# Kernel tuning notes

Hardware: AMD Instinct MI355X
Metric: run time of the kernel (lower is better)

Reference implementation:

```python
import jax, jax.numpy as jnp
import numpy as np

INPUT_SIZE = 512.0
NMS_THRESH = 0.3
SCORE_THRESH = 0.5
TOPC = 256        # candidates entering NMS (top-scoring above-threshold boxes)
MAX_DETS = 32     # py_cpu_nms(...)[:32]


def conv3x3(x, w):
    return jax.lax.conv_general_dilated(x, w, (1, 1), 'SAME',
                                        dimension_numbers=('NCHW', 'OIHW', 'NCHW'))


def bn_eval(x, g, b, m, v, eps=1e-5):
    inv = g * jax.lax.rsqrt(v + eps)
    return x * inv[None, :, None, None] + (b - m * inv)[None, :, None, None]


def lrelu(x):
    return jnp.where(x >= 0, x, 0.01 * x)


def upsample2x(x):  # F.interpolate(scale_factor=2), default nearest
    return jnp.repeat(jnp.repeat(x, 2, axis=2), 2, axis=3)


def fpn_head(x, hw1, hg1, hb1, hm1, hv1, hw2, hg2, hb2, hm2, hv2):
    x = lrelu(bn_eval(conv3x3(x, hw1), hg1, hb1, hm1, hv1))
    x = lrelu(bn_eval(conv3x3(x, hw2), hg2, hb2, hm2, hv2))
    return x


def decode_boxes(t, a):
    # inverse of coordinate_change: x1 = ax1 + tx*aw, w = aw*exp(tw)
    aw = a[:, 2] - a[:, 0]
    ah = a[:, 3] - a[:, 1]
    x1 = a[:, 0] + t[:, 0] * aw
    y1 = a[:, 1] + t[:, 1] * ah
    bw = aw * jnp.exp(t[:, 2])
    bh = ah * jnp.exp(t[:, 3])
    return jnp.stack([x1, y1, x1 + bw, y1 + bh], axis=1)


def pairwise_iou_p1(b):
    # py_cpu_nms convention: +1 in widths/areas
    x1, y1, x2, y2 = b[:, 0], b[:, 1], b[:, 2], b[:, 3]
    areas = (x2 - x1 + 1.0) * (y2 - y1 + 1.0)
    xx1 = jnp.maximum(x1[:, None], x1[None, :])
    yy1 = jnp.maximum(y1[:, None], y1[None, :])
    xx2 = jnp.minimum(x2[:, None], x2[None, :])
    yy2 = jnp.minimum(y2[:, None], y2[None, :])
    inter = jnp.maximum(0.0, xx2 - xx1 + 1.0) * jnp.maximum(0.0, yy2 - yy1 + 1.0)
    return inter / (areas[:, None] + areas[None, :] - inter)


def nms_keep(boxes, valid):
    # boxes pre-sorted by descending score; greedy suppression
    ovr = pairwise_iou_p1(boxes)
    idxs = jnp.arange(boxes.shape[0])

    def body(i, keep):
        sup = (ovr[i] > NMS_THRESH) & (idxs > i) & keep[i]
        return keep & ~sup

    return jax.lax.fori_loop(0, boxes.shape[0], body, valid)


def roi_adaptive_maxpool(feat, c):
    # feat [C,h,w]; c = [x1,y1,x2,y2] int32 feature-map coords
    # faithful F.adaptive_max_pool2d(feat[:, y1:y2, x1:x2], (7,7))
    C, h, w = feat.shape
    neg = jnp.finfo(feat.dtype).min

    def bin_masks(lo, hi, n_axis):
        L = hi - lo
        i = jnp.arange(7)
        start = (i * L) // 7
        end = ((i + 1) * L + 6) // 7  # ceil
        rel = jnp.arange(n_axis) - lo
        return (rel[None, :] >= start[:, None]) & (rel[None, :] < end[:, None])

    my = bin_masks(c[1], c[3], h)  # [7,h]
    mx = bin_masks(c[0], c[2], w)  # [7,w]
    rows = jnp.stack([jnp.max(jnp.where(my[i][None, :, None], feat, neg), axis=1)
                      for i in range(7)])                    # [7y,C,w]
    cols = jnp.stack([jnp.max(jnp.where(mx[j][None, None, :], rows, neg), axis=2)
                      for j in range(7)])
    return cols.transpose(2, 1, 0)


def rpn_level(feat, anchors, stride, clsw, locw):
    B = feat.shape[0]
    score = jax.nn.sigmoid(conv3x3(feat, clsw)).transpose(0, 2, 3, 1).reshape(B, -1)
    loc = conv3x3(feat, locw).transpose(0, 2, 3, 1).reshape(B, -1, 4)

    def per_image(f, sc, t):
        boxes = jnp.clip(decode_boxes(t, anchors), 0.0, INPUT_SIZE)
        bw = boxes[:, 2] - boxes[:, 0]
        bh = boxes[:, 3] - boxes[:, 1]
        valid = (sc > SCORE_THRESH) & (bw >= 2.0 * stride) & (bh >= 2.0 * stride)
        vals, idx = jax.lax.top_k(jnp.where(valid, sc, -1.0), TOPC)
        cb = boxes[idx]
        # original NMS ran on detached numpy -> stop_gradient
        keep = nms_keep(jax.lax.stop_gradient(cb), vals > SCORE_THRESH)
        order = jnp.argsort(jnp.where(keep, 0, 1), stable=True)[:MAX_DETS]
        m = keep[order]
        b32 = cb[order]
        s32 = vals[order]
        coords = jnp.where(m[:, None], b32.astype(jnp.int32) // stride,
                           jnp.array([0, 0, 2, 2], jnp.int32))
        pooled = jax.vmap(lambda cc: roi_adaptive_maxpool(f, cc))(coords)
        pooled = jnp.where(m[:, None, None, None], pooled, 0.0)
        dets = jnp.where(m[:, None], jnp.concatenate([b32, s32[:, None]], axis=1), 0.0)
        return dets, m, pooled

    return jax.vmap(per_image)(feat, score, loc)


def net_forward(layer2, layer3, layer4, anchors2, anchors3, anchors4,
                hw1, hg1, hb1, hm1, hv1, hw2, hg2, hb2, hm2, hv2, clsw, locw):
    head = (hw1, hg1, hb1, hm1, hv1, hw2, hg2, hb2, hm2, hv2)
    l3 = layer3 + upsample2x(layer4)
    l2 = layer2 + upsample2x(l3)
    f2 = fpn_head(l2, *head)
    f3 = fpn_head(l3, *head)
    f4 = fpn_head(layer4, *head)
    outs = [rpn_level(f, a, s, clsw, locw)
            for f, a, s in ((f2, anchors2, 8), (f3, anchors3, 16), (f4, anchors4, 32))]
    dets = jnp.stack([o[0] for o in outs], axis=1)  # [B,3,32,5] padded eval_test
    mask = jnp.stack([o[1] for o in outs], axis=1)  # [B,3,32] validity of each det
    rois = jnp.stack([o[2] for o in outs], axis=1)  # [B,3,32,256,7,7]
    return dets, mask, rois


def setup_inputs() -> dict:
    key = jax.random.key(0)
    ks = jax.random.split(key, 16)
    f32 = jnp.float32

    def n(k, shape, s=1.0):
        return jax.random.normal(k, shape, f32) * s

    S = 512

    def anchors_for(st):
        h = S // st
        c = (jnp.arange(h, dtype=f32) + 0.5) * st
        sz = jnp.array([4.0, 6.0, 8.0], f32) * st
        cy = jnp.broadcast_to(c[:, None, None], (h, h, 3))
        cx = jnp.broadcast_to(c[None, :, None], (h, h, 3))
        ss = jnp.broadcast_to(sz[None, None, :], (h, h, 3))
        return jnp.stack([cx - ss / 2, cy - ss / 2, cx + ss / 2, cy + ss / 2], -1).reshape(-1, 4)

    return {
        'layer2': n(ks[0], (2, 256, 64, 64)),
        'layer3': n(ks[1], (2, 256, 32, 32)),
        'layer4': n(ks[2], (2, 256, 16, 16)),
        'anchors2': anchors_for(8),
        'anchors3': anchors_for(16),
        'anchors4': anchors_for(32),
        'hw1': n(ks[3], (256, 256, 3, 3), 0.03),
        'hg1': 1.0 + n(ks[4], (256,), 0.1),
        'hb1': n(ks[5], (256,), 0.1),
        'hm1': n(ks[6], (256,), 0.1),
        'hv1': jax.random.uniform(ks[7], (256,), f32, 0.5, 1.5),
        'hw2': n(ks[8], (256, 256, 3, 3), 0.03),
        'hg2': 1.0 + n(ks[9], (256,), 0.1),
        'hb2': n(ks[10], (256,), 0.1),
        'hm2': n(ks[11], (256,), 0.1),
        'hv2': jax.random.uniform(ks[12], (256,), f32, 0.5, 1.5),
        'clsw': n(ks[13], (3, 256, 3, 3), 0.03),
        'locw': n(ks[14], (12, 256, 3, 3), 0.01),
    }


def reference(layer2, layer3, layer4, anchors2, anchors3, anchors4,
              hw1, hg1, hb1, hm1, hv1, hw2, hg2, hb2, hm2, hv2, clsw, locw):
    return net_forward(layer2, layer3, layer4, anchors2, anchors3, anchors4,
                       hw1, hg1, hb1, hm1, hv1, hw2, hg2, hb2, hm2, hv2, clsw, locw)
```

## Files before the change

kernel.cpp:

```cpp
#include <hip/hip_runtime.h>
#include <math.h>

typedef __attribute__((ext_vector_type(8))) _Float16 f16x8;
typedef __attribute__((ext_vector_type(16))) float f32x16;
typedef unsigned long long ull;

__device__ __forceinline__ void split2(float v, _Float16& h, _Float16& l) {
  h = (_Float16)v;
  l = (_Float16)((v - (float)h) * 4096.0f);
}

#define OFF_W1H  0UL
#define OFF_W1L  1179648UL
#define OFF_W2H  2359296UL
#define OFF_W2L  3538944UL
#define OFF_WRH  4718592UL
#define OFF_WRL  4866048UL
#define OFF_I0H  5013504UL
#define OFF_I0L  9207808UL
#define OFF_I1H  13402112UL
#define OFF_I1L  14450688UL
#define OFF_I2H  15499264UL
#define OFF_I2L  15761408UL
#define OFF_L3F  16023552UL
#define OFF_H0H  18120704UL
#define OFF_H0L  22315008UL
#define OFF_H1H  26509312UL
#define OFF_H1L  27557888UL
#define OFF_H2H  28606464UL
#define OFF_H2L  28868608UL
#define OFF_LOGITS 29130752UL
#define OFF_TVALS  29259776UL
#define OFF_SKEY   29775872UL
#define OFF_COORDS 29904896UL
#define OFF_BN     29908992UL
#define OFF_HIST   29917184UL
#define OFF_P0     29966336UL
#define WS_NEED2   51986432UL


__global__ __launch_bounds__(256) void zero_hist_kernel(unsigned int* __restrict__ hist)
{
  hist[blockIdx.x * 256 + threadIdx.x] = 0u;
}

#define L1SZ 589824
#define RPNSZ 73728
__global__ __launch_bounds__(256) void prep_w_kernel(
    const float* __restrict__ hw1, const float* __restrict__ hw2,
    const float* __restrict__ clsw, const float* __restrict__ locw,
    const float* __restrict__ hg1, const float* __restrict__ hb1,
    const float* __restrict__ hm1, const float* __restrict__ hv1,
    const float* __restrict__ hg2, const float* __restrict__ hb2,
    const float* __restrict__ hm2, const float* __restrict__ hv2,
    char* __restrict__ ws)
{
  if (blockIdx.x == 0) {
    int t = threadIdx.x;
    float* inv1 = (float*)(ws + OFF_BN);
    float* beta1 = inv1 + 256;
    float* inv2 = inv1 + 512;
    float* beta2 = inv1 + 768;
    float i1 = (float)((double)hg1[t] / sqrt((double)hv1[t] + 1e-5));
    inv1[t] = i1;
    beta1[t] = hb1[t] - hm1[t] * i1;
    float i2 = (float)((double)hg2[t] / sqrt((double)hv2[t] + 1e-5));
    inv2[t] = i2;
    beta2[t] = hb2[t] - hm2[t] * i2;
  }
  _Float16* w1h = (_Float16*)(ws + OFF_W1H);
  _Float16* w1l = (_Float16*)(ws + OFF_W1L);
  _Float16* w2h = (_Float16*)(ws + OFF_W2H);
  _Float16* w2l = (_Float16*)(ws + OFF_W2L);
  _Float16* wrh = (_Float16*)(ws + OFF_WRH);
  _Float16* wrl = (_Float16*)(ws + OFF_WRL);
  const int TOT = 2 * L1SZ + RPNSZ;
  for (int e = blockIdx.x * 256 + threadIdx.x; e < TOT; e += gridDim.x * 256) {
    float val; _Float16 *dh, *dl; int di;
    if (e < L1SZ) {
      int dydx = e >> 16, oc = (e >> 8) & 255, ic = e & 255;
      val = hw1[(size_t)(oc * 256 + ic) * 9 + dydx];
      dh = w1h; dl = w1l; di = e;
    } else if (e < 2 * L1SZ) {
      int e2 = e - L1SZ;
      int dydx = e2 >> 16, oc = (e2 >> 8) & 255, ic = e2 & 255;
      val = hw2[(size_t)(oc * 256 + ic) * 9 + dydx];
      dh = w2h; dl = w2l; di = e2;
    } else {
      int e3 = e - 2 * L1SZ;
      int dydx = e3 >> 13, oc = (e3 >> 8) & 31, ic = e3 & 255;
      if (oc < 3) val = clsw[(size_t)(oc * 256 + ic) * 9 + dydx];
      else if (oc < 15) val = locw[(size_t)((oc - 3) * 256 + ic) * 9 + dydx];
      else val = 0.f;
      dh = wrh; dl = wrl; di = e3;
    }
    _Float16 h, l;
    split2(val, h, l);
    dh[di] = h; dl[di] = l;
  }
}

__global__ __launch_bounds__(256) void fuse_kernel(
    const float* __restrict__ a, const float* __restrict__ bUp,
    float* __restrict__ f32chw, _Float16* __restrict__ oH, _Float16* __restrict__ oL,
    int H, int logW)
{
  __shared__ float T[32][65];
  int HW = H * H;
  int img = blockIdx.y;
  const float* ap = a + (size_t)img * 256 * HW;
  const float* bp = bUp ? (bUp + (size_t)img * 256 * (HW >> 2)) : nullptr;
  float* fp = f32chw ? (f32chw + (size_t)img * 256 * HW) : nullptr;
  _Float16* oHp = oH + (size_t)img * HW * 256;
  _Float16* oLp = oL + (size_t)img * HW * 256;
  int p0 = blockIdx.x * 64;
  int tid = threadIdx.x;
  int px = tid & 63, cg = tid >> 6;
  int gp = p0 + px;
  int y = gp >> logW, x = gp & (H - 1);
  int px2 = tid >> 2, q = tid & 3;
  for (int c0 = 0; c0 < 256; c0 += 32) {
    #pragma unroll
    for (int cc = 0; cc < 8; ++cc) {
      int c = c0 + cg * 8 + cc;
      float v = ap[(size_t)c * HW + gp];
      if (bp) v += bp[(size_t)c * (HW >> 2) + (y >> 1) * (H >> 1) + (x >> 1)];
      if (fp) fp[(size_t)c * HW + gp] = v;
      T[cg * 8 + cc][px] = v;
    }
    __syncthreads();
    {
      size_t oa = (size_t)(p0 + px2) * 256 + c0 + q * 8;
      f16x8 hs, ls;
      #pragma unroll
      for (int j = 0; j < 8; ++j) {
        float v = T[q * 8 + j][px2];
        _Float16 h, l;
        split2(v, h, l);
        hs[j] = h; ls[j] = l;
      }
      *(f16x8*)&oHp[oa] = hs;
      *(f16x8*)&oLp[oa] = ls;
    }
    __syncthreads();
  }
}

struct CArgs {
  const _Float16* inH[3]; const _Float16* inL[3];
  const _Float16* wH; const _Float16* wL;
  _Float16* outH[3]; _Float16* outL[3];
  const float* inv; const float* beta;
  float* logits; float* tvals;
  float* pbase; size_t pstride;
  int mode; int parts;
};

#define PXS 42

template<int OCW, int WN, int NI>
__global__ __launch_bounds__(WN * 64, 2) void conv_mfma_kernel(CArgs a)
{
  constexpr int NT = WN * 64;
  constexpr int NOC = WN * NI * 32;
  constexpr int OCG = OCW / NOC;
  __shared__ _Float16 Ph[2][100 * PXS], Pl[2][100 * PXS];

  int bt = blockIdx.x;
  int lvl, tile;
  if (bt < 64) { lvl = 0; tile = bt; }
  else if (bt < 80) { lvl = 1; tile = bt - 64; }
  else { lvl = 2; tile = bt - 80; }
  int H = (lvl == 0) ? 64 : ((lvl == 1) ? 32 : 16);
  int HW = H * H;
  int tpr = H >> 3;
  int ty0 = (tile / tpr) * 8, tx0 = (tile % tpr) * 8;
  int img = blockIdx.z;

  int part = blockIdx.y / OCG;
  int ocb = (blockIdx.y % OCG) * NOC;
  int nicb = 8 / a.parts;
  int icb0 = part * nicb;
  float* pout = (a.parts > 1) ? (a.pbase + (size_t)part * a.pstride) : nullptr;

  const _Float16* inH = a.inH[lvl] + (size_t)img * HW * 256;
  const _Float16* inL = a.inL[lvl] + (size_t)img * HW * 256;

  int tid = threadIdx.x;
  int lane = tid & 63, wn = tid >> 6;
  int row = lane & 31, khalf = lane >> 5;
  int abase[2];
  #pragma unroll
  for (int mi = 0; mi < 2; ++mi) {
    int m = mi * 32 + row;
    abase[mi] = ((m >> 3) * 10 + (m & 7)) * PXS + khalf * 8;
  }

  const _Float16* wHb = a.wH + (size_t)(ocb + wn * NI * 32 + row) * 256 + khalf * 8 + icb0 * 32;
  const _Float16* wLb = a.wL + (size_t)(ocb + wn * NI * 32 + row) * 256 + khalf * 8 + icb0 * 32;

  f32x16 acc1[2][NI], acc2[2][NI];
  #pragma unroll
  for (int mi = 0; mi < 2; ++mi)
    #pragma unroll
    for (int ni = 0; ni < NI; ++ni)
      #pragma unroll
      for (int j = 0; j < 16; ++j) { acc1[mi][ni][j] = 0.f; acc2[mi][ni][j] = 0.f; }

  auto stage = [&](int icb, int buf) {
    for (int u = tid; u < 400; u += NT) {
      int pxl = u >> 2, icq = u & 3;
      int py = pxl / 10, pxx = pxl - py * 10;
      int gy = ty0 + py - 1, gx = tx0 + pxx - 1;
      int lo = pxl * PXS + icq * 8;
      if ((unsigned)gy < (unsigned)H && (unsigned)gx < (unsigned)H) {
        size_t ga = (size_t)(gy * H + gx) * 256 + icb * 32 + icq * 8;
        *(f16x8*)&Ph[buf][lo] = *(const f16x8*)&inH[ga];
        *(f16x8*)&Pl[buf][lo] = *(const f16x8*)&inL[ga];
      } else {
        f16x8 z;
        #pragma unroll
        for (int j = 0; j < 8; ++j) z[j] = (_Float16)0.f;
        *(f16x8*)&Ph[buf][lo] = z;
        *(f16x8*)&Pl[buf][lo] = z;
      }
    }
  };

  stage(icb0, 0);
  __syncthreads();

  for (int rel = 0; rel < nicb; ++rel) {
    int cur = rel & 1;
    if (rel < nicb - 1) stage(icb0 + rel + 1, cur ^ 1);
    #pragma unroll
    for (int dydx = 0; dydx < 9; ++dydx) {
      int sh = ((dydx / 3) * 10 + (dydx % 3)) * PXS;
      #pragma unroll
      for (int k2 = 0; k2 < 2; ++k2) {
        f16x8 bh[NI], bl[NI], ah[2], al[2];
        #pragma unroll
        for (int ni = 0; ni < NI; ++ni) {
          size_t ga = (size_t)dydx * OCW * 256 + (size_t)ni * 32 * 256 + rel * 32 + k2 * 16;
          bh[ni] = *(const f16x8*)&wHb[ga];
          bl[ni] = *(const f16x8*)&wLb[ga];
        }
        #pragma unroll
        for (int mi = 0; mi < 2; ++mi) {
          int off = abase[mi] + sh + k2 * 16;
          ah[mi] = *(const f16x8*)&Ph[cur][off];
          al[mi] = *(const f16x8*)&Pl[cur][off];
        }
        __builtin_amdgcn_s_setprio(1);
        #pragma unroll
        for (int mi = 0; mi < 2; ++mi)
          #pragma unroll
          for (int ni = 0; ni < NI; ++ni) {
            acc1[mi][ni] = __builtin_amdgcn_mfma_f32_32x32x16_f16(ah[mi], bh[ni], acc1[mi][ni], 0, 0, 0);
            acc2[mi][ni] = __builtin_amdgcn_mfma_f32_32x32x16_f16(ah[mi], bl[ni], acc2[mi][ni], 0, 0, 0);
            acc2[mi][ni] = __builtin_amdgcn_mfma_f32_32x32x16_f16(al[mi], bh[ni], acc2[mi][ni], 0, 0, 0);
          }
        __builtin_amdgcn_s_setprio(0);
      }
    }
    __syncthreads();
  }

  int poffv = (lvl == 0) ? 0 : ((lvl == 1) ? 4096 : 5120);
  #pragma unroll
  for (int mi = 0; mi < 2; ++mi)
    #pragma unroll
    for (int ni = 0; ni < NI; ++ni) {
      int oc = ocb + wn * NI * 32 + ni * 32 + row;
      float v[16];
      #pragma unroll
      for (int r = 0; r < 16; ++r) v[r] = acc1[mi][ni][r] + acc2[mi][ni][r] * (1.f / 4096.f);
      if (pout) {
        float* pp = pout + (size_t)(img * 5376 + poffv) * OCW;
        #pragma unroll
        for (int r = 0; r < 16; ++r) {
          int ml = (r & 3) + 8 * (r >> 2) + 4 * khalf;
          int m = mi * 32 + ml;
          int y = ty0 + (m >> 3), x = tx0 + (m & 7);
          pp[(size_t)(y * H + x) * OCW + oc] = v[r];
        }
      } else if (a.mode == 0) {
        _Float16* outH = a.outH[lvl] + (size_t)img * HW * 256;
        _Float16* outL = a.outL[lvl] + (size_t)img * HW * 256;
        float iv = a.inv[oc], bb = a.beta[oc];
        #pragma unroll
        for (int r = 0; r < 16; ++r) {
          int ml = (r & 3) + 8 * (r >> 2) + 4 * khalf;
          int m = mi * 32 + ml;
          int y = ty0 + (m >> 3), x = tx0 + (m & 7);
          float vv = v[r] * iv + bb;
          vv = (vv >= 0.f) ? vv : 0.01f * vv;
          _Float16 h, l;
          split2(vv, h, l);
          size_t oa = (size_t)(y * H + x) * 256 + oc;
          outH[oa] = h;
          outL[oa] = l;
        }
      } else {
        if (oc < 15) {
          int abse = (lvl == 0) ? 0 : ((lvl == 1) ? 12288 : 15360);
          #pragma unroll
          for (int r = 0; r < 16; ++r) {
            int ml = (r & 3) + 8 * (r >> 2) + 4 * khalf;
            int m = mi * 32 + ml;
            int y = ty0 + (m >> 3), x = tx0 + (m & 7);
            int gi = img * 16128 + abse + (y * H + x) * 3;
            if (oc < 3) a.logits[gi + oc] = v[r];
            else { int r2 = oc - 3; a.tvals[(size_t)(gi + (r2 >> 2)) * 4 + (r2 & 3)] = v[r]; }
          }
        }
      }
    }
}

__global__ __launch_bounds__(256) void combine_head_kernel(
    const float* __restrict__ pb, int nparts,
    const float* __restrict__ inv, const float* __restrict__ beta,
    _Float16* __restrict__ oH0, _Float16* __restrict__ oL0,
    _Float16* __restrict__ oH1, _Float16* __restrict__ oL1,
    _Float16* __restrict__ oH2, _Float16* __restrict__ oL2)
{
  const size_t PS = 10752UL * 256UL;
  int g = blockIdx.x * 256 + threadIdx.x;
  int pixel = g >> 5, q = g & 31;
  size_t base = (size_t)pixel * 256 + q * 8;
  int img = pixel / 5376, rem = pixel - img * 5376;
  int lvl = (rem < 4096) ? 0 : ((rem < 5120) ? 1 : 2);
  int poffv = (lvl == 0) ? 0 : ((lvl == 1) ? 4096 : 5120);
  int HW = (lvl == 0) ? 4096 : ((lvl == 1) ? 1024 : 256);
  int lpx = rem - poffv;
  size_t oa = ((size_t)img * HW + lpx) * 256 + q * 8;
  _Float16* oH = ((lvl == 0) ? oH0 : ((lvl == 1) ? oH1 : oH2)) + oa;
  _Float16* oL = ((lvl == 0) ? oL0 : ((lvl == 1) ? oL1 : oL2)) + oa;
  f16x8 hs, ls;
  #pragma unroll
  for (int j = 0; j < 8; ++j) {
    int oc = q * 8 + j;
    float s = 0.f;
    for (int k = 0; k < nparts; ++k) s += pb[(size_t)k * PS + base + j];
    float vv = s * inv[oc] + beta[oc];
    vv = (vv >= 0.f) ? vv : 0.01f * vv;
    _Float16 h, l;
    split2(vv, h, l);
    hs[j] = h; ls[j] = l;
  }
  *(f16x8*)oH = hs;
  *(f16x8*)oL = ls;
}

__global__ __launch_bounds__(256) void combine_rpn_kernel(
    const float* __restrict__ praw, int nparts,
    float* __restrict__ logits, float* __restrict__ tvals)
{
  int g = blockIdx.x * 256 + threadIdx.x;
  int px = g >> 4, oc = g & 15;
  if (oc == 15) return;
  float s = 0.f;
  for (int p = 0; p < nparts; ++p) s += praw[((size_t)p * 10752 + px) * 32 + oc];
  int img = px / 5376, rem = px - img * 5376;
  int lvl = (rem < 4096) ? 0 : ((rem < 5120) ? 1 : 2);
  int poffv = (lvl == 0) ? 0 : ((lvl == 1) ? 4096 : 5120);
  int abase = (lvl == 0) ? 0 : ((lvl == 1) ? 12288 : 15360);
  int gi = img * 16128 + abase + (rem - poffv) * 3;
  if (oc < 3) logits[gi + oc] = s;
  else { int r2 = oc - 3; tvals[(size_t)(gi + (r2 >> 2)) * 4 + (r2 & 3)] = s; }
}

__device__ __forceinline__ void decode_one(const float* __restrict__ anch,
                                           const float* __restrict__ tv, int i,
                                           float& x1, float& y1, float& x2, float& y2)
{
  float t0 = tv[i * 4 + 0], t1 = tv[i * 4 + 1], t2 = tv[i * 4 + 2], t3 = tv[i * 4 + 3];
  float a0 = anch[i * 4 + 0], a1 = anch[i * 4 + 1], a2 = anch[i * 4 + 2], a3 = anch[i * 4 + 3];
  float aw = a2 - a0, ah = a3 - a1;
  float xx = a0 + t0 * aw;
  float yy = a1 + t1 * ah;
  float bw = aw * expf(t2);
  float bh = ah * expf(t3);
  x1 = fminf(fmaxf(xx, 0.f), 512.f);
  y1 = fminf(fmaxf(yy, 0.f), 512.f);
  x2 = fminf(fmaxf(xx + bw, 0.f), 512.f);
  y2 = fminf(fmaxf(yy + bh, 0.f), 512.f);
}

__global__ __launch_bounds__(256) void score_kernel(
    const float* __restrict__ logits, const float* __restrict__ tvals,
    const float* __restrict__ anch0, const float* __restrict__ anch1, const float* __restrict__ anch2,
    unsigned int* __restrict__ skey, unsigned int* __restrict__ hist)
{
  int g = blockIdx.x * 256 + threadIdx.x;
  if (g >= 2 * 16128) return;
  int img = g / 16128, r = g - img * 16128;
  int lvl = (r < 12288) ? 0 : ((r < 15360) ? 1 : 2);
  int abase = (lvl == 0) ? 0 : ((lvl == 1) ? 12288 : 15360);
  int stride = (lvl == 0) ? 8 : ((lvl == 1) ? 16 : 32);
  const float* anch = (lvl == 0) ? anch0 : ((lvl == 1) ? anch1 : anch2);
  int i = r - abase;
  float lv = logits[g];
  float sc = 1.f / (1.f + expf(-lv));
  float x1, y1, x2, y2;
  decode_one(anch, tvals + (size_t)(img * 16128 + abase) * 4, i, x1, y1, x2, y2);
  float minsz = 2.0f * (float)stride;
  bool valid = (sc > 0.5f) && ((x2 - x1) >= minsz) && ((y2 - y1) >= minsz);
  unsigned int key = valid ? __float_as_uint(sc) : 0u;
  skey[g] = key;
  if (valid)
    atomicAdd(&hist[(img * 3 + lvl) * 2048 + ((key & 0xFFFFFFu) >> 13)], 1u);
}

__global__ __launch_bounds__(256) void postproc_kernel(
    const float* __restrict__ tvals,
    const float* __restrict__ anch0, const float* __restrict__ anch1, const float* __restrict__ anch2,
    const unsigned int* __restrict__ skey, const unsigned int* __restrict__ hist,
    float* __restrict__ dout, int* __restrict__ coords)
{
  int lvl = blockIdx.x, img = blockIdx.y;
  int N = (lvl == 0) ? 12288 : ((lvl == 1) ? 3072 : 768);
  int stride = (lvl == 0) ? 8 : ((lvl == 1) ? 16 : 32);
  int abase = (lvl == 0) ? 0 : ((lvl == 1) ? 12288 : 15360);
  const float* anch = (lvl == 0) ? anch0 : ((lvl == 1) ? anch1 : anch2);
  const float* tv = tvals + (size_t)(img * 16128 + abase) * 4;
  const unsigned int* sk = skey + img * 16128 + abase;
  int tx = threadIdx.x;

  __shared__ int tot[256];
  __shared__ int sh_bin, sh_V;
  __shared__ ull slist[1024];
  __shared__ int scnt;
  __shared__ ull skey64[256];
  __shared__ float bx0[256], bx1[256], bx2[256], bx3[256], bar[256], bsc[256];
  __shared__ ull colT[256][4];
  __shared__ ull kinit[4], kfin[4];
  __shared__ unsigned char bkeepArr[256];
  __shared__ int sel[32];

  const unsigned int* hp = hist + (img * 3 + lvl) * 2048;
  unsigned int hloc[8];
  #pragma unroll
  for (int j = 0; j < 8; ++j) hloc[j] = hp[tx * 8 + j];
  int sl[9]; sl[8] = 0;
  #pragma unroll
  for (int j = 7; j >= 0; --j) sl[j] = sl[j + 1] + (int)hloc[j];
  tot[tx] = sl[0];
  if (tx == 0) { sh_bin = 2048; scnt = 0; }
  __syncthreads();
  int T = 0;
  for (int b = 0; b < 256; ++b) T += (b > tx) ? tot[b] : 0;
  if (tx == 0) sh_V = T + sl[0];
  __syncthreads();
  int V = sh_V;
  int needed = (V < 256) ? V : 256;
  if (needed > 0) {
    #pragma unroll
    for (int j = 0; j < 8; ++j) {
      int suf = T + sl[j];
      int sufn = (j < 7) ? (T + sl[j + 1]) : T;
      if (suf >= needed && sufn < needed) sh_bin = tx * 8 + j;
    }
  }
  #pragma unroll
  for (int q = 0; q < 4; ++q) slist[tx + q * 256] = 0ull;
  __syncthreads();
  int Bstar = sh_bin;

  if (needed > 0) {
    const uint4* sk4 = (const uint4*)sk;
    for (int i4 = tx; i4 < (N >> 2); i4 += 256) {
      uint4 v4 = sk4[i4];
      unsigned int vv[4] = {v4.x, v4.y, v4.z, v4.w};
      #pragma unroll
      for (int q = 0; q < 4; ++q) {
        unsigned int v = vv[q];
        if (v != 0u && (int)((v & 0xFFFFFFu) >> 13) >= Bstar) {
          int p = atomicAdd(&scnt, 1);
          if (p < 1024)
            slist[p] = ((ull)v << 32) | (ull)(0xFFFFFFFFu - (unsigned)(i4 * 4 + q));
        }
      }
    }
  }
  __syncthreads();
  int M = scnt < 1024 ? scnt : 1024;

  skey64[tx] = 0ull;
  __syncthreads();
  for (int it = tx; it < M; it += 256) {
    ull K = slist[it];
    int rank = 0;
    for (int j = 0; j < M; ++j) rank += (slist[j] > K) ? 1 : 0;
    if (rank < 256) skey64[rank] = K;
  }
  __syncthreads();

  {
    ull key = skey64[tx];
    float x1 = 0.f, y1 = 0.f, x2 = 0.f, y2 = 0.f, sc = 0.f;
    if (key != 0ull) {
      sc = __uint_as_float((unsigned int)(key >> 32));
      int idx = (int)(0xFFFFFFFFu - (unsigned int)(key & 0xFFFFFFFFull));
      decode_one(anch, tv, idx, x1, y1, x2, y2);
    }
    bx0[tx] = x1; bx1[tx] = y1; bx2[tx] = x2; bx3[tx] = y2;
    bsc[tx] = sc;
    bar[tx] = (x2 - x1 + 1.f) * (y2 - y1 + 1.f);
    ull b = __ballot(sc > 0.5f);
    if ((tx & 63) == 0) kinit[tx >> 6] = b;
  }
  __syncthreads();

  {
    float xj1 = bx0[tx], yj1 = bx1[tx], xj2 = bx2[tx], yj2 = bx3[tx], aj = bar[tx];
    #pragma unroll
    for (int w = 0; w < 4; ++w) {
      ull rr = 0ull;
      int j0 = w * 64;
      int ie = (tx < j0 + 64) ? tx : (j0 + 64);
      for (int i = j0; i < ie; ++i) {
        float xx1 = fmaxf(xj1, bx0[i]);
        float yy1 = fmaxf(yj1, bx1[i]);
        float xx2 = fminf(xj2, bx2[i]);
        float yy2 = fminf(yj2, bx3[i]);
        float ww = fmaxf(0.f, xx2 - xx1 + 1.f);
        float hh = fmaxf(0.f, yy2 - yy1 + 1.f);
        float inter = ww * hh;
        float ovr = inter / (aj + bar[i] - inter);
        rr |= (ovr > 0.3f) ? (1ull << (i & 63)) : 0ull;
      }
      colT[tx][w] = rr;
    }
  }
  __syncthreads();

  if (tx < 64) {
    int l = tx;
    ull cm[4][4];
    #pragma unroll
    for (int c = 0; c < 4; ++c)
      #pragma unroll
      for (int w = 0; w < 4; ++w) cm[c][w] = colT[l + 64 * c][w];
    int av[4];
    #pragma unroll
    for (int c = 0; c < 4; ++c) av[c] = (int)((kinit[c] >> l) & 1ull);
    for (int cw = 0; cw < 4; ++cw) {
      ull rem = __ballot(av[cw] != 0);
      while (rem) {
        int ib = __builtin_ctzll(rem);
        #pragma unroll
        for (int c = 0; c < 4; ++c) {
          int sup = (int)((cm[c][cw] >> ib) & 1ull);
          av[c] &= sup ^ 1;
        }
        ull ready = __ballot(av[cw] != 0);
        rem = (ib == 63) ? 0ull : (ready & (~0ull << (ib + 1)));
      }
    }
    #pragma unroll
    for (int c = 0; c < 4; ++c) {
      ull bw = __ballot(av[c] != 0);
      if (l == 0) kfin[c] = bw;
      bkeepArr[l + 64 * c] = (unsigned char)av[c];
    }
  }
  __syncthreads();

  {
    int r = tx;
    int m = bkeepArr[r];
    int K = 0, before = 0;
    #pragma unroll
    for (int c = 0; c < 4; ++c) {
      int pc = __popcll(kfin[c]);
      K += pc;
      if (r >= (c + 1) * 64) before += pc;
      else if (r > c * 64) before += __popcll(kfin[c] & ((1ull << (r - c * 64)) - 1ull));
    }
    int rank = m ? before : (K + r - before);
    if (rank < 32) sel[rank] = r;
  }
  __syncthreads();

  if (tx < 32) {
    int r = sel[tx];
    int m = bkeepArr[r];
    int ob = (img * 3 + lvl) * 32 + tx;
    float d0 = 0.f, d1 = 0.f, d2 = 0.f, d3 = 0.f, d4 = 0.f;
    int c0 = 0, c1 = 0, c2 = 2, c3 = 2;
    if (m) {
      d0 = bx0[r]; d1 = bx1[r]; d2 = bx2[r]; d3 = bx3[r]; d4 = bsc[r];
      c0 = ((int)d0) / stride; c1 = ((int)d1) / stride;
      c2 = ((int)d2) / stride; c3 = ((int)d3) / stride;
    }
    dout[ob * 5 + 0] = d0; dout[ob * 5 + 1] = d1; dout[ob * 5 + 2] = d2;
    dout[ob * 5 + 3] = d3; dout[ob * 5 + 4] = d4;
    dout[960 + ob] = m ? 1.f : 0.f;
    coords[ob * 5 + 0] = c0; coords[ob * 5 + 1] = c1;
    coords[ob * 5 + 2] = c2; coords[ob * 5 + 3] = c3;
    coords[ob * 5 + 4] = m;
  }
}

__global__ __launch_bounds__(256) void roipool_kernel(
    const _Float16* __restrict__ fh0, const _Float16* __restrict__ fl0,
    const _Float16* __restrict__ fh1, const _Float16* __restrict__ fl1,
    const _Float16* __restrict__ fh2, const _Float16* __restrict__ fl2,
    const int* __restrict__ coords, float* __restrict__ dout)
{
  int bx = blockIdx.x;
  int slot = bx / 49, bin = bx - slot * 49;
  int yi = bin / 7, xi = bin - yi * 7;
  int lvl = blockIdx.y, img = blockIdx.z;
  int ob = (img * 3 + lvl) * 32 + slot;
  int c = threadIdx.x;
  const int* cw = coords + ob * 5;
  float* outp = dout + 1152 + (size_t)ob * 256 * 49 + (size_t)c * 49 + yi * 7 + xi;
  int m = cw[4];
  if (!m) { *outp = 0.f; return; }
  int H = (lvl == 0) ? 64 : ((lvl == 1) ? 32 : 16);
  const _Float16* fh = ((lvl == 0) ? fh0 : ((lvl == 1) ? fh1 : fh2)) + (size_t)img * H * H * 256;
  const _Float16* fl = ((lvl == 0) ? fl0 : ((lvl == 1) ? fl1 : fl2)) + (size_t)img * H * H * 256;
  int lox = cw[0], loy = cw[1], hix = cw[2], hiy = cw[3];
  int Lx = hix - lox, Ly = hiy - loy;
  int ys = loy + (yi * Ly) / 7;
  int ye = loy + ((yi + 1) * Ly + 6) / 7;
  int xs = lox + (xi * Lx) / 7;
  int xe = lox + ((xi + 1) * Lx + 6) / 7;
  float mx = -3.402823466e+38f;
  for (int y = ys; y < ye; ++y) {
    size_t rowb = ((size_t)y * H) * 256 + c;
    for (int x = xs; x < xe; ++x) {
      size_t idx = rowb + (size_t)x * 256;
      float v = (float)fh[idx] + (float)fl[idx] * (1.f / 4096.f);
      mx = fmaxf(mx, v);
    }
  }
  *outp = mx;
}

extern "C" void kernel_launch(void* const* d_in, const int* in_sizes, int n_in,
                              void* d_out, int out_size, void* d_ws, size_t ws_size,
                              hipStream_t stream)
{
  (void)in_sizes; (void)n_in; (void)out_size;
  char* ws = (char*)d_ws;
  const float* layer2 = (const float*)d_in[0];
  const float* layer3 = (const float*)d_in[1];
  const float* layer4 = (const float*)d_in[2];
  const float* anch2  = (const float*)d_in[3];
  const float* anch3  = (const float*)d_in[4];
  const float* anch4  = (const float*)d_in[5];
  const float* hw1 = (const float*)d_in[6];
  const float* hg1 = (const float*)d_in[7];
  const float* hb1 = (const float*)d_in[8];
  const float* hm1 = (const float*)d_in[9];
  const float* hv1 = (const float*)d_in[10];
  const float* hw2 = (const float*)d_in[11];
  const float* hg2 = (const float*)d_in[12];
  const float* hb2 = (const float*)d_in[13];
  const float* hm2 = (const float*)d_in[14];
  const float* hv2 = (const float*)d_in[15];
  const float* clsw = (const float*)d_in[16];
  const float* locw = (const float*)d_in[17];
  float* dout = (float*)d_out;

  int hparts = (ws_size >= WS_NEED2) ? 2 : 1;
  int rparts = (ws_size >= WS_NEED2) ? 8 : 1;

  _Float16* i0H = (_Float16*)(ws + OFF_I0H);
  _Float16* i0L = (_Float16*)(ws + OFF_I0L);
  _Float16* i1H = (_Float16*)(ws + OFF_I1H);
  _Float16* i1L = (_Float16*)(ws + OFF_I1L);
  _Float16* i2H = (_Float16*)(ws + OFF_I2H);
  _Float16* i2L = (_Float16*)(ws + OFF_I2L);
  float* l3f = (float*)(ws + OFF_L3F);
  _Float16* h0H = (_Float16*)(ws + OFF_H0H);
  _Float16* h0L = (_Float16*)(ws + OFF_H0L);
  _Float16* h1H = (_Float16*)(ws + OFF_H1H);
  _Float16* h1L = (_Float16*)(ws + OFF_H1L);
  _Float16* h2H = (_Float16*)(ws + OFF_H2H);
  _Float16* h2L = (_Float16*)(ws + OFF_H2L);
  float* logits = (float*)(ws + OFF_LOGITS);
  float* tvals  = (float*)(ws + OFF_TVALS);
  unsigned int* skey = (unsigned int*)(ws + OFF_SKEY);
  int* coords = (int*)(ws + OFF_COORDS);
  float* bn = (float*)(ws + OFF_BN);
  float* inv1 = bn; float* beta1 = bn + 256; float* inv2 = bn + 512; float* beta2 = bn + 768;
  unsigned int* hist = (unsigned int*)(ws + OFF_HIST);
  float* P0 = (float*)(ws + OFF_P0);

  zero_hist_kernel<<<48, 256, 0, stream>>>(hist);
  prep_w_kernel<<<2048, 256, 0, stream>>>(hw1, hw2, clsw, locw,
                                          hg1, hb1, hm1, hv1, hg2, hb2, hm2, hv2, ws);

  fuse_kernel<<<dim3(4, 2), 256, 0, stream>>>(layer4, nullptr, nullptr, i2H, i2L, 16, 4);
  fuse_kernel<<<dim3(16, 2), 256, 0, stream>>>(layer3, layer4, l3f, i1H, i1L, 32, 5);
  fuse_kernel<<<dim3(64, 2), 256, 0, stream>>>(layer2, l3f, nullptr, i0H, i0L, 64, 6);

  CArgs c1;
  c1.inH[0] = i0H; c1.inH[1] = i1H; c1.inH[2] = i2H;
  c1.inL[0] = i0L; c1.inL[1] = i1L; c1.inL[2] = i2L;
  c1.wH = (const _Float16*)(ws + OFF_W1H); c1.wL = (const _Float16*)(ws + OFF_W1L);
  c1.outH[0] = h0H; c1.outH[1] = h1H; c1.outH[2] = h2H;
  c1.outL[0] = h0L; c1.outL[1] = h1L; c1.outL[2] = h2L;
  c1.inv = inv1; c1.beta = beta1;
  c1.logits = nullptr; c1.tvals = nullptr;
  c1.pbase = P0; c1.pstride = 10752UL * 256UL;
  c1.mode = 0; c1.parts = hparts;
  conv_mfma_kernel<256, 2, 2><<<dim3(84, hparts * 2, 2), 128, 0, stream>>>(c1);
  if (hparts > 1)
    combine_head_kernel<<<1344, 256, 0, stream>>>(P0, hparts, inv1, beta1,
                                                  h0H, h0L, h1H, h1L, h2H, h2L);

  _Float16* f0H = i0H; _Float16* f0L = i0L;
  _Float16* f1H = i1H; _Float16* f1L = i1L;
  _Float16* f2H = i2H; _Float16* f2L = i2L;

  CArgs c2;
  c2.inH[0] = h0H; c2.inH[1] = h1H; c2.inH[2] = h2H;
  c2.inL[0] = h0L; c2.inL[1] = h1L; c2.inL[2] = h2L;
  c2.wH = (const _Float16*)(ws + OFF_W2H); c2.wL = (const _Float16*)(ws + OFF_W2L);
  c2.outH[0] = f0H; c2.outH[1] = f1H; c2.outH[2] = f2H;
  c2.outL[0] = f0L; c2.outL[1] = f1L; c2.outL[2] = f2L;
  c2.inv = inv2; c2.beta = beta2;
  c2.logits = nullptr; c2.tvals = nullptr;
  c2.pbase = P0; c2.pstride = 10752UL * 256UL;
  c2.mode = 0; c2.parts = hparts;
  conv_mfma_kernel<256, 2, 2><<<dim3(84, hparts * 2, 2), 128, 0, stream>>>(c2);
  if (hparts > 1)
    combine_head_kernel<<<1344, 256, 0, stream>>>(P0, hparts, inv2, beta2,
                                                  f0H, f0L, f1H, f1L, f2H, f2L);

  CArgs cr;
  cr.inH[0] = f0H; cr.inH[1] = f1H; cr.inH[2] = f2H;
  cr.inL[0] = f0L; cr.inL[1] = f1L; cr.inL[2] = f2L;
  cr.wH = (const _Float16*)(ws + OFF_WRH); cr.wL = (const _Float16*)(ws + OFF_WRL);
  cr.outH[0] = nullptr; cr.outH[1] = nullptr; cr.outH[2] = nullptr;
  cr.outL[0] = nullptr; cr.outL[1] = nullptr; cr.outL[2] = nullptr;
  cr.inv = nullptr; cr.beta = nullptr;
  cr.logits = logits; cr.tvals = tvals;
  cr.pbase = P0; cr.pstride = 10752UL * 32UL;
  cr.mode = 2; cr.parts = rparts;
  conv_mfma_kernel<32, 1, 1><<<dim3(84, rparts, 2), 64, 0, stream>>>(cr);
  if (rparts > 1)
    combine_rpn_kernel<<<672, 256, 0, stream>>>(P0, rparts, logits, tvals);

  score_kernel<<<126, 256, 0, stream>>>(logits, tvals, anch2, anch3, anch4, skey, hist);
  postproc_kernel<<<dim3(3, 2), 256, 0, stream>>>(tvals, anch2, anch3, anch4, skey, hist, dout, coords);
  roipool_kernel<<<dim3(32 * 49, 3, 2), 256, 0, stream>>>(f0H, f0L, f1H, f1L, f2H, f2L, coords, dout);
}
```

Measured before the change: 369.2 us.

## Merge small launches, change LDS padding, drop setprio, halve RPN split parts

Folds histogram zeroing into the weight-prep kernel and merges the two small-level fuse launches into one, which removes two kernel launches. It also changes the LDS row stride from 42 to 40 halves, removes the s_setprio hints around the MFMA block, and reduces the RPN split-K part count from 8 to 4. The stride of 40 may bring back LDS bank conflicts, and fewer RPN parts lowers parallelism while also cutting combine work.

```diff
diff --git a/kernel.cpp b/kernel.cpp
--- a/kernel.cpp
+++ b/kernel.cpp
@@ -39,11 +39,6 @@
 #define WS_NEED2   51986432UL
 
 
-__global__ __launch_bounds__(256) void zero_hist_kernel(unsigned int* __restrict__ hist)
-{
-  hist[blockIdx.x * 256 + threadIdx.x] = 0u;
-}
-
 #define L1SZ 589824
 #define RPNSZ 73728
 __global__ __launch_bounds__(256) void prep_w_kernel(
@@ -67,6 +62,8 @@
     float i2 = (float)((double)hg2[t] / sqrt((double)hv2[t] + 1e-5));
     inv2[t] = i2;
     beta2[t] = hb2[t] - hm2[t] * i2;
+  } else if (blockIdx.x <= 48) {
+    ((unsigned int*)(ws + OFF_HIST))[(blockIdx.x - 1) * 256 + threadIdx.x] = 0u;
   }
   _Float16* w1h = (_Float16*)(ws + OFF_W1H);
   _Float16* w1l = (_Float16*)(ws + OFF_W1L);
@@ -100,20 +97,19 @@
   }
 }
 
-__global__ __launch_bounds__(256) void fuse_kernel(
+__device__ __forceinline__ void fuse_body(
+    float T[32][65],
     const float* __restrict__ a, const float* __restrict__ bUp,
     float* __restrict__ f32chw, _Float16* __restrict__ oH, _Float16* __restrict__ oL,
-    int H, int logW)
-{
-  __shared__ float T[32][65];
+    int H, int logW, int bx, int img)
+{
   int HW = H * H;
-  int img = blockIdx.y;
   const float* ap = a + (size_t)img * 256 * HW;
   const float* bp = bUp ? (bUp + (size_t)img * 256 * (HW >> 2)) : nullptr;
   float* fp = f32chw ? (f32chw + (size_t)img * 256 * HW) : nullptr;
   _Float16* oHp = oH + (size_t)img * HW * 256;
   _Float16* oLp = oL + (size_t)img * HW * 256;
-  int p0 = blockIdx.x * 64;
+  int p0 = bx * 64;
   int tid = threadIdx.x;
   int px = tid & 63, cg = tid >> 6;
   int gp = p0 + px;
@@ -146,6 +142,29 @@
   }
 }
 
+__global__ __launch_bounds__(256) void fuse_small_kernel(
+    const float* __restrict__ layer4, const float* __restrict__ layer3,
+    float* __restrict__ l3f,
+    _Float16* __restrict__ i2H, _Float16* __restrict__ i2L,
+    _Float16* __restrict__ i1H, _Float16* __restrict__ i1L)
+{
+  __shared__ float T[32][65];
+  int img = blockIdx.y;
+  if (blockIdx.x < 4)
+    fuse_body(T, layer4, nullptr, nullptr, i2H, i2L, 16, 4, blockIdx.x, img);
+  else
+    fuse_body(T, layer3, layer4, l3f, i1H, i1L, 32, 5, blockIdx.x - 4, img);
+}
+
+__global__ __launch_bounds__(256) void fuse_kernel(
+    const float* __restrict__ a, const float* __restrict__ bUp,
+    float* __restrict__ f32chw, _Float16* __restrict__ oH, _Float16* __restrict__ oL,
+    int H, int logW)
+{
+  __shared__ float T[32][65];
+  fuse_body(T, a, bUp, f32chw, oH, oL, H, logW, blockIdx.x, blockIdx.y);
+}
+
 struct CArgs {
   const _Float16* inH[3]; const _Float16* inL[3];
   const _Float16* wH; const _Float16* wL;
@@ -156,7 +175,7 @@
   int mode; int parts;
 };
 
-#define PXS 42
+#define PXS 40
 
 template<int OCW, int WN, int NI>
 __global__ __launch_bounds__(WN * 64, 2) void conv_mfma_kernel(CArgs a)
@@ -251,7 +270,6 @@
           ah[mi] = *(const f16x8*)&Ph[cur][off];
           al[mi] = *(const f16x8*)&Pl[cur][off];
         }
-        __builtin_amdgcn_s_setprio(1);
         #pragma unroll
         for (int mi = 0; mi < 2; ++mi)
           #pragma unroll
@@ -260,7 +278,6 @@
             acc2[mi][ni] = __builtin_amdgcn_mfma_f32_32x32x16_f16(ah[mi], bl[ni], acc2[mi][ni], 0, 0, 0);
             acc2[mi][ni] = __builtin_amdgcn_mfma_f32_32x32x16_f16(al[mi], bh[ni], acc2[mi][ni], 0, 0, 0);
           }
-        __builtin_amdgcn_s_setprio(0);
       }
     }
     __syncthreads();
@@ -668,7 +685,7 @@
   float* dout = (float*)d_out;
 
   int hparts = (ws_size >= WS_NEED2) ? 2 : 1;
-  int rparts = (ws_size >= WS_NEED2) ? 8 : 1;
+  int rparts = (ws_size >= WS_NEED2) ? 4 : 1;
 
   _Float16* i0H = (_Float16*)(ws + OFF_I0H);
   _Float16* i0L = (_Float16*)(ws + OFF_I0L);
@@ -692,12 +709,10 @@
   unsigned int* hist = (unsigned int*)(ws + OFF_HIST);
   float* P0 = (float*)(ws + OFF_P0);
 
-  zero_hist_kernel<<<48, 256, 0, stream>>>(hist);
   prep_w_kernel<<<2048, 256, 0, stream>>>(hw1, hw2, clsw, locw,
                                           hg1, hb1, hm1, hv1, hg2, hb2, hm2, hv2, ws);
 
-  fuse_kernel<<<dim3(4, 2), 256, 0, stream>>>(layer4, nullptr, nullptr, i2H, i2L, 16, 4);
-  fuse_kernel<<<dim3(16, 2), 256, 0, stream>>>(layer3, layer4, l3f, i1H, i1L, 32, 5);
+  fuse_small_kernel<<<dim3(20, 2), 256, 0, stream>>>(layer4, layer3, l3f, i2H, i2L, i1H, i1L);
   fuse_kernel<<<dim3(64, 2), 256, 0, stream>>>(layer2, l3f, nullptr, i0H, i0L, 64, 6);
 
   CArgs c1;
```

After: 342.2 us. 7.3% less time.
